# Kernel tuning notes

Measured on AMD Instinct MI355X. Metric: run time of the kernel, lower is better.

The kernel has to match this reference:

```python
import jax, jax.numpy as jnp
from jax import lax
import numpy as np

EPS = 1e-5

def _bn(y, g, b):
    # train-mode batchnorm over (B, H, W) per channel, biased variance (torch default)
    m = y.mean(axis=(0, 2, 3), keepdims=True)
    v = y.var(axis=(0, 2, 3), keepdims=True)
    return (y - m) * lax.rsqrt(v + EPS) * g[None, :, None, None] + b[None, :, None, None]

def _pool13(y):
    # max_pool2d kernel (13,1), stride (13,1); torch truncates the remainder
    B, Ch, L, C = y.shape
    L2 = (L // 13) * 13
    return y[:, :, :L2, :].reshape(B, Ch, L // 13, 13, C).max(axis=3)

def _stagenet(x, w1, b1, w2, b2, g1, be1, w3, b3, g2, be2, wl, bl):
    # x: (B, T=3000, C) -> (B, 100)
    B = x.shape[0]
    y = jnp.einsum('btc,oc->bot', x, w1) + b1[None, :, None]   # spatial conv across channels
    y = y.transpose(0, 2, 1)[:, None]                          # (B,1,T,C)
    y = lax.conv_general_dilated(y, w2, (1, 1), 'VALID', dimension_numbers=('NCHW', 'OIHW', 'NCHW')) + b2[None, :, None, None]
    y = _pool13(_bn(jax.nn.relu(y), g1, be1))                  # (B,16,227,C)
    y = lax.conv_general_dilated(y, w3, (1, 1), 'VALID', dimension_numbers=('NCHW', 'OIHW', 'NCHW')) + b3[None, :, None, None]
    y = _pool13(_bn(jax.nn.relu(y), g2, be2))                  # (B,16,13,C)
    return y.reshape(B, -1) @ wl.T + bl                        # (B,100)

def _gru_last(xs, wih, whh, bih, bhh):
    # xs: (B, S, D) -> final hidden state (B, H); torch gate order r, z, n
    h0 = jnp.zeros((xs.shape[0], whh.shape[1]), xs.dtype)
    def step(h, x):
        gi = x @ wih.T + bih
        gh = h @ whh.T + bhh
        ir, iz, inn = jnp.split(gi, 3, axis=-1)
        hr, hz, hnn = jnp.split(gh, 3, axis=-1)
        r = jax.nn.sigmoid(ir + hr)
        z = jax.nn.sigmoid(iz + hz)
        n = jnp.tanh(inn + r * hnn)
        return (1.0 - z) * n + z * h, None
    hT, _ = lax.scan(step, h0, xs.transpose(1, 0, 2))
    return hT

def setup_inputs() -> dict:
    key = jax.random.key(0)
    ks = jax.random.split(key, 16)
    B, Np, Nb, T, C, H = 16, 16, 10, 3000, 2, 100
    s = 0.1
    f32 = jnp.float32
    return {
        'Xc': jax.random.normal(ks[0], (B, Np, T, C), f32),
        'Xp': jax.random.normal(ks[1], (B, Np, T, C), f32),
        'Xb': jax.random.normal(ks[2], (B, Np, Nb, T, C), f32),
        'sn_w1': jax.random.normal(ks[3], (C, C), f32) * s,
        'sn_b1': jnp.zeros((C,), f32),
        'sn_w2': jax.random.normal(ks[4], (16, 1, 50, 1), f32) * s,
        'sn_b2': jnp.zeros((16,), f32),
        'sn_g1': jnp.ones((16,), f32),
        'sn_be1': jnp.zeros((16,), f32),
        'sn_w3': jax.random.normal(ks[5], (16, 16, 50, 1), f32) * s,
        'sn_b3': jnp.zeros((16,), f32),
        'sn_g2': jnp.ones((16,), f32),
        'sn_be2': jnp.zeros((16,), f32),
        'sn_wl': jax.random.normal(ks[6], (H, 16 * 13 * C), f32) * s,
        'sn_bl': jnp.zeros((H,), f32),
        'gru_wih': jax.random.normal(ks[7], (3 * H, H), f32) * s,
        'gru_whh': jax.random.normal(ks[8], (3 * H, H), f32) * s,
        'gru_bih': jnp.zeros((3 * H,), f32),
        'gru_bhh': jnp.zeros((3 * H,), f32),
        'bilin_w': jax.random.normal(ks[9], (Np, H, H), f32) * s,
    }

def reference(Xc, Xp, Xb, sn_w1, sn_b1, sn_w2, sn_b2, sn_g1, sn_be1, sn_w3, sn_b3, sn_g2, sn_be2, sn_wl, sn_bl, gru_wih, gru_whh, gru_bih, gru_bhh, bilin_w):
    sn = lambda x: _stagenet(x, sn_w1, sn_b1, sn_w2, sn_b2, sn_g1, sn_be1, sn_w3, sn_b3, sn_g2, sn_be2, sn_wl, sn_bl)
    B, Np, Nb, T, C = Xb.shape
    # each original stagenet call sees one window with batch B (BN stats per call) -> vmap over windows
    xb = jax.vmap(sn)(Xb.transpose(1, 2, 0, 3, 4).reshape(Np * Nb, B, T, C))
    xb = xb.reshape(Np, Nb, B, -1).transpose(2, 0, 1, 3)            # (B,Np,Nb,100)
    xc = jax.vmap(sn)(Xc.transpose(1, 0, 2, 3)).transpose(1, 0, 2)  # (B,S,100)
    xp = jax.vmap(sn)(Xp.transpose(1, 0, 2, 3)).transpose(1, 0, 2)  # (B,Np,100)
    hn = _gru_last(xc, gru_wih, gru_whh, gru_bih, gru_bhh)          # (B,100)
    cand = jnp.concatenate([xp[:, :, None, :], xb], axis=2)         # (B,Np,Nb+1,100)
    # per-step bilinear scoring: replaces the triple nested loop of nn.Bilinear calls
    return jnp.einsum('bh,phc,bpsc->bps', hn, bilin_w, cand)        # (B,16,11)
```

## Files before the change

kernel.cpp:

```cpp
#include <hip/hip_runtime.h>
#include <hip/hip_bf16.h>


#define NSEQ 3072
#define CNT1 94432.0f
#define CNT2 5696.0f

__global__ __launch_bounds__(256) void k0_prep(
    const float* __restrict__ wl, const float* __restrict__ w3,
    const float* __restrict__ wih, const float* __restrict__ whh,
    float* __restrict__ wlT, float* __restrict__ w3T,
    float* __restrict__ wihT, float* __restrict__ whhT)
{
    int i = blockIdx.x * 256 + threadIdx.x;
    if (i < 41600) { int h = i / 416, c = i - h * 416; wlT[c * 100 + h] = wl[i]; }
    if (i < 12800) { int co = i / 800, r = i - co * 800; int ci = r / 50, k = r - ci * 50;
                     w3T[(ci * 50 + k) * 16 + co] = w3[i]; }
    if (i < 30000) { int j = i / 100, c = i - j * 100;
                     wihT[c * 300 + j] = wih[i]; whhT[c * 300 + j] = whh[i]; }
}

__global__ __launch_bounds__(256) void k1(
    const float* __restrict__ Xc, const float* __restrict__ Xp, const float* __restrict__ Xb,
    const float* __restrict__ w1, const float* __restrict__ b1,
    const float* __restrict__ w2, const float* __restrict__ b2,
    const float* __restrict__ g1,
    float* __restrict__ pooled1, float* __restrict__ bp1)
{
    const int s = blockIdx.x;
    const int g = s >> 4, b = s & 15;
    const float* x;
    if (g < 160)      { int p = g / 10, nb = g - p * 10; x = Xb + (size_t)((b * 16 + p) * 10 + nb) * 6000; }
    else if (g < 176) { int p = g - 160; x = Xc + (size_t)(b * 16 + p) * 6000; }
    else              { int p = g - 176; x = Xp + (size_t)(b * 16 + p) * 6000; }

    __shared__ float u[6000];
    __shared__ float w2s[800];
    __shared__ float red[512];
    const int tid = threadIdx.x;

    for (int i = tid; i < 800; i += 256) w2s[i] = w2[i];
    float w100 = w1[0], w101 = w1[1], w110 = w1[2], w111 = w1[3];
    float b10 = b1[0], b11 = b1[1];
    for (int t = tid; t < 3000; t += 256) {
        float x0 = x[t * 2], x1 = x[t * 2 + 1];
        u[t * 2]     = fmaf(x1, w101, fmaf(x0, w100, b10));
        u[t * 2 + 1] = fmaf(x1, w111, fmaf(x0, w110, b11));
    }
    __syncthreads();

    const int pair = tid & 31, ch = pair >> 1, col = pair & 1, w8 = tid >> 5;
    float wk[50];
    #pragma unroll
    for (int k = 0; k < 50; ++k) wk[k] = w2s[ch * 50 + k];
    const float bias = b2[ch];
    const bool useMax = (g1[ch] >= 0.0f);

    float lsum = 0.0f, lsq = 0.0f;
    #pragma unroll 1
    for (int w = w8; w < 227; w += 8) {
        const int t0 = w * 13;
        float acc[13];
        #pragma unroll
        for (int j = 0; j < 13; ++j) acc[j] = bias;
        #pragma unroll
        for (int tk = 0; tk < 62; ++tk) {
            float uv = u[(t0 + tk) * 2 + col];
            const int jlo = (tk > 49) ? (tk - 49) : 0;
            const int jhi = (tk < 12) ? tk : 12;
            #pragma unroll
            for (int j = 0; j < 13; ++j)
                if (j >= jlo && j <= jhi) acc[j] = fmaf(uv, wk[tk - j], acc[j]);
        }
        float sel = useMax ? -1e30f : 1e30f;
        #pragma unroll
        for (int j = 0; j < 13; ++j) {
            float r = fmaxf(acc[j], 0.0f);
            lsum += r; lsq = fmaf(r, r, lsq);
            sel = useMax ? fmaxf(sel, r) : fminf(sel, r);
        }
        pooled1[(size_t)s * 7264 + (size_t)w * 32 + pair] = sel;
    }

    red[tid] = lsum;
    __syncthreads();
    float partial_sq = lsq;
    if (tid < 16) {
        float a = 0.0f;
        for (int t = 0; t < 16; ++t) { int idx = (t >> 1) * 32 + tid * 2 + (t & 1); a += red[idx]; }
        bp1[(s * 16 + tid) * 2 + 0] = a;
    }
    __syncthreads();
    red[tid] = partial_sq;
    __syncthreads();
    if (tid < 16) {
        float q = 0.0f;
        for (int t = 0; t < 16; ++t) { int idx = (t >> 1) * 32 + tid * 2 + (t & 1); q += red[idx]; }
        bp1[(s * 16 + tid) * 2 + 1] = q;
    }
}

__global__ __launch_bounds__(512) void k2(
    const float* __restrict__ pooled1, const float* __restrict__ bp1,
    const float* __restrict__ g1, const float* __restrict__ be1,
    const float* __restrict__ w3T, const float* __restrict__ b3,
    const float* __restrict__ g2,
    float* __restrict__ pooled2, float* __restrict__ bp2)
{
    const int s = blockIdx.x, g = s >> 4;
    __shared__ float in2[7424];
    __shared__ float w3b[800];
    __shared__ float sc1[16], sh1[16];
    __shared__ float red[1024];
    const int tid = threadIdx.x;

    if (tid < 16) {
        float sum = 0.0f, sq = 0.0f;
        for (int sb = 0; sb < 16; ++sb) {
            const float* pp = &bp1[((g * 16 + sb) * 16 + tid) * 2];
            sum += pp[0]; sq += pp[1];
        }
        float m = sum * (1.0f / CNT1);
        float v = sq * (1.0f / CNT1) - m * m;
        float scv = g1[tid] * rsqrtf(v + 1e-5f);
        sc1[tid] = scv; sh1[tid] = be1[tid] - m * scv;
    }
    for (int i = tid; i < 7424; i += 512) in2[i] = 0.0f;
    __syncthreads();
    for (int idx = tid; idx < 7264; idx += 512) {
        int w = idx >> 5, pr = idx & 31, ch = pr >> 1, cl = pr & 1;
        in2[(cl * 16 + ch) * 232 + w] = fmaf(pooled1[(size_t)s * 7264 + idx], sc1[ch], sh1[ch]);
    }

    const int pair = tid & 31, co = pair >> 1, col = pair & 1, wslot = tid >> 5;
    const bool active = (wslot < 14);
    const int t0 = wslot * 13;
    float acc[13];
    const float bias = b3[co];
    #pragma unroll
    for (int j = 0; j < 13; ++j) acc[j] = bias;

    for (int ci = 0; ci < 16; ++ci) {
        __syncthreads();
        for (int i = tid; i < 800; i += 512) w3b[i] = w3T[ci * 800 + i];
        __syncthreads();
        if (active) {
            float wk[50];
            #pragma unroll
            for (int k = 0; k < 50; ++k) wk[k] = w3b[k * 16 + co];
            const float* ip = &in2[(col * 16 + ci) * 232 + t0];
            #pragma unroll
            for (int tk = 0; tk < 62; ++tk) {
                float uv = ip[tk];
                const int jlo = (tk > 49) ? (tk - 49) : 0;
                const int jhi = (tk < 12) ? tk : 12;
                #pragma unroll
                for (int j = 0; j < 13; ++j)
                    if (j >= jlo && j <= jhi) acc[j] = fmaf(uv, wk[tk - j], acc[j]);
            }
        }
    }

    float lsum = 0.0f, lsq = 0.0f;
    const bool useMax2 = (g2[co] >= 0.0f);
    float sel = useMax2 ? -1e30f : 1e30f;
    if (active) {
        const int base = wslot * 13;
        #pragma unroll
        for (int j = 0; j < 13; ++j) {
            if (base + j < 178) {
                float r = fmaxf(acc[j], 0.0f);
                lsum += r; lsq = fmaf(r, r, lsq);
                sel = useMax2 ? fmaxf(sel, r) : fminf(sel, r);
            }
        }
        if (wslot < 13) pooled2[(size_t)s * 416 + co * 26 + wslot * 2 + col] = sel;
    }
    red[tid] = lsum; red[512 + tid] = lsq;
    __syncthreads();
    if (tid < 16) {
        float a = 0.0f, q = 0.0f;
        for (int t = 0; t < 32; ++t) {
            int idx = (t >> 1) * 32 + tid * 2 + (t & 1);
            a += red[idx]; q += red[512 + idx];
        }
        bp2[(s * 16 + tid) * 2 + 0] = a;
        bp2[(s * 16 + tid) * 2 + 1] = q;
    }
}

__global__ __launch_bounds__(128) void k3(
    const float* __restrict__ bp2, const float* __restrict__ g2, const float* __restrict__ be2,
    const float* __restrict__ pooled2, const float* __restrict__ wlT,
    const float* __restrict__ bl, float* __restrict__ feat)
{
    const int s = blockIdx.x, g = s >> 4;
    const int tid = threadIdx.x;
    __shared__ float sc[16], sh[16], z[416];
    if (tid < 16) {
        float sum = 0.0f, sq = 0.0f;
        for (int sb = 0; sb < 16; ++sb) {
            const float* pp = &bp2[((g * 16 + sb) * 16 + tid) * 2];
            sum += pp[0]; sq += pp[1];
        }
        float m = sum * (1.0f / CNT2);
        float v = sq * (1.0f / CNT2) - m * m;
        float scv = g2[tid] * rsqrtf(v + 1e-5f);
        sc[tid] = scv; sh[tid] = be2[tid] - m * scv;
    }
    __syncthreads();
    for (int i = tid; i < 416; i += 128) {
        int co = i / 26;
        z[i] = fmaf(pooled2[(size_t)s * 416 + i], sc[co], sh[co]);
    }
    __syncthreads();
    for (int h = tid; h < 100; h += 128) {
        float acc = bl[h];
        for (int i = 0; i < 416; ++i) acc = fmaf(wlT[i * 100 + h], z[i], acc);
        feat[(size_t)s * 100 + h] = acc;
    }
}

__global__ __launch_bounds__(128) void k4a(
    const float* __restrict__ feat, const float* __restrict__ wihT,
    const float* __restrict__ bih, float* __restrict__ gi)
{
    const int b = blockIdx.x >> 4, p = blockIdx.x & 15;
    const int tid = threadIdx.x;
    __shared__ float xr[100];
    if (tid < 100) xr[tid] = feat[(size_t)((160 + p) * 16 + b) * 100 + tid];
    __syncthreads();
    for (int j = tid; j < 300; j += 128) {
        float acc = bih[j];
        for (int i = 0; i < 100; ++i) acc = fmaf(xr[i], wihT[i * 300 + j], acc);
        gi[(size_t)(b * 16 + p) * 300 + j] = acc;
    }
}

__global__ __launch_bounds__(320) void k4b(
    const float* __restrict__ gi, const float* __restrict__ whhT,
    const float* __restrict__ bhh, float* __restrict__ hn)
{
    const int b = blockIdx.x;
    const int tid = threadIdx.x;
    __shared__ float h[100], ga[300], gb[300];
    if (tid < 100) h[tid] = 0.0f;
    __syncthreads();
    for (int p = 0; p < 16; ++p) {
        if (tid < 300) {
            float acc = bhh[tid];
            for (int i = 0; i < 100; ++i) acc = fmaf(h[i], whhT[i * 300 + tid], acc);
            gb[tid] = acc;
            ga[tid] = gi[(size_t)(b * 16 + p) * 300 + tid];
        }
        __syncthreads();
        if (tid < 100) {
            float r  = 1.0f / (1.0f + expf(-(ga[tid] + gb[tid])));
            float zz = 1.0f / (1.0f + expf(-(ga[100 + tid] + gb[100 + tid])));
            float n  = tanhf(ga[200 + tid] + r * gb[200 + tid]);
            h[tid] = (1.0f - zz) * n + zz * h[tid];
        }
        __syncthreads();
    }
    if (tid < 100) hn[b * 100 + tid] = h[tid];
}

__global__ __launch_bounds__(128) void k5(
    const float* __restrict__ hn, const float* __restrict__ bw,
    const float* __restrict__ feat, float* __restrict__ out)
{
    const int b = blockIdx.x >> 4, p = blockIdx.x & 15;
    const int tid = threadIdx.x;
    __shared__ float hs[100], ts[100];
    if (tid < 100) hs[tid] = hn[b * 100 + tid];
    __syncthreads();
    if (tid < 100) {
        float acc = 0.0f;
        for (int hh = 0; hh < 100; ++hh)
            acc = fmaf(hs[hh], bw[(size_t)(p * 100 + hh) * 100 + tid], acc);
        ts[tid] = acc;
    }
    __syncthreads();
    if (tid < 11) {
        const float* cr = (tid == 0)
            ? &feat[(size_t)((176 + p) * 16 + b) * 100]
            : &feat[(size_t)((p * 10 + tid - 1) * 16 + b) * 100];
        float acc = 0.0f;
        for (int hh = 0; hh < 100; ++hh) acc = fmaf(ts[hh], cr[hh], acc);
        out[(b * 16 + p) * 11 + tid] = acc;
    }
}

extern "C" void kernel_launch(void* const* d_in, const int* in_sizes, int n_in,
                              void* d_out, int out_size, void* d_ws, size_t ws_size,
                              hipStream_t stream) {
    (void)in_sizes; (void)n_in; (void)out_size; (void)ws_size;
    const float* Xc  = (const float*)d_in[0];
    const float* Xp  = (const float*)d_in[1];
    const float* Xb  = (const float*)d_in[2];
    const float* w1  = (const float*)d_in[3];
    const float* b1  = (const float*)d_in[4];
    const float* w2  = (const float*)d_in[5];
    const float* b2  = (const float*)d_in[6];
    const float* g1  = (const float*)d_in[7];
    const float* be1 = (const float*)d_in[8];
    const float* w3  = (const float*)d_in[9];
    const float* b3  = (const float*)d_in[10];
    const float* g2  = (const float*)d_in[11];
    const float* be2 = (const float*)d_in[12];
    const float* wl  = (const float*)d_in[13];
    const float* bl  = (const float*)d_in[14];
    const float* wih = (const float*)d_in[15];
    const float* whh = (const float*)d_in[16];
    const float* bih = (const float*)d_in[17];
    const float* bhh = (const float*)d_in[18];
    const float* bw  = (const float*)d_in[19];

    float* ws      = (float*)d_ws;
    float* bp1     = ws;
    float* bp2     = ws + 98304;
    float* wlT     = ws + 196608;
    float* w3T     = ws + 238208;
    float* wihT    = ws + 251008;
    float* whhT    = ws + 281008;
    float* gi      = ws + 311008;
    float* hn      = ws + 387808;
    float* feat    = ws + 389408;
    float* pooled2 = ws + 696608;
    float* pooled1 = ws + 1974560;

    k0_prep<<<163, 256, 0, stream>>>(wl, w3, wih, whh, wlT, w3T, wihT, whhT);
    k1<<<NSEQ, 256, 0, stream>>>(Xc, Xp, Xb, w1, b1, w2, b2, g1, pooled1, bp1);
    k2<<<NSEQ, 512, 0, stream>>>(pooled1, bp1, g1, be1, w3T, b3, g2, pooled2, bp2);
    k3<<<NSEQ, 128, 0, stream>>>(bp2, g2, be2, pooled2, wlT, bl, feat);
    k4a<<<256, 128, 0, stream>>>(feat, wihT, bih, gi);
    k4b<<<16, 320, 0, stream>>>(gi, whhT, bhh, hn);
    k5<<<256, 128, 0, stream>>>(hn, bw, feat, (float*)d_out);
}
```

Before: 762.5 us.

## Double-buffer conv3 weights, trim idle warps, vectorize input loads in conv kernels

In k2 the per-input-channel weight slice is now double-buffered in shared memory, so the next slice is prefetched while the current one is used. This removes one of the two barriers per channel iteration. The block shrinks from 512 to 448 threads, dropping the two idle warps, and only the padding tail of the input buffer is zeroed instead of all of it. k1 loads and writes its channel-mix input with float4, and both kernels pin the weight registers with empty asm statements to keep the compiler from rematerializing them.

```diff
diff --git a/kernel.cpp b/kernel.cpp
--- a/kernel.cpp
+++ b/kernel.cpp
@@ -34,7 +34,7 @@
     else if (g < 176) { int p = g - 160; x = Xc + (size_t)(b * 16 + p) * 6000; }
     else              { int p = g - 176; x = Xp + (size_t)(b * 16 + p) * 6000; }
 
-    __shared__ float u[6000];
+    __shared__ __align__(16) float u[6000];
     __shared__ float w2s[800];
     __shared__ float red[512];
     const int tid = threadIdx.x;
@@ -42,10 +42,14 @@
     for (int i = tid; i < 800; i += 256) w2s[i] = w2[i];
     float w100 = w1[0], w101 = w1[1], w110 = w1[2], w111 = w1[3];
     float b10 = b1[0], b11 = b1[1];
-    for (int t = tid; t < 3000; t += 256) {
-        float x0 = x[t * 2], x1 = x[t * 2 + 1];
-        u[t * 2]     = fmaf(x1, w101, fmaf(x0, w100, b10));
-        u[t * 2 + 1] = fmaf(x1, w111, fmaf(x0, w110, b11));
+    for (int t4 = tid; t4 < 1500; t4 += 256) {
+        float4 xv = ((const float4*)x)[t4];
+        float4 uv;
+        uv.x = fmaf(xv.y, w101, fmaf(xv.x, w100, b10));
+        uv.y = fmaf(xv.y, w111, fmaf(xv.x, w110, b11));
+        uv.z = fmaf(xv.w, w101, fmaf(xv.z, w100, b10));
+        uv.w = fmaf(xv.w, w111, fmaf(xv.z, w110, b11));
+        ((float4*)u)[t4] = uv;
     }
     __syncthreads();
 
@@ -53,6 +57,8 @@
     float wk[50];
     #pragma unroll
     for (int k = 0; k < 50; ++k) wk[k] = w2s[ch * 50 + k];
+    #pragma unroll
+    for (int k = 0; k < 50; ++k) asm volatile("" : "+v"(wk[k]));
     const float bias = b2[ch];
     const bool useMax = (g1[ch] >= 0.0f);
 
@@ -100,7 +106,7 @@
     }
 }
 
-__global__ __launch_bounds__(512) void k2(
+__global__ __launch_bounds__(448) void k2(
     const float* __restrict__ pooled1, const float* __restrict__ bp1,
     const float* __restrict__ g1, const float* __restrict__ be1,
     const float* __restrict__ w3T, const float* __restrict__ b3,
@@ -109,9 +115,9 @@
 {
     const int s = blockIdx.x, g = s >> 4;
     __shared__ float in2[7424];
-    __shared__ float w3b[800];
+    __shared__ float w3b[2][800];
     __shared__ float sc1[16], sh1[16];
-    __shared__ float red[1024];
+    __shared__ float red[896];
     const int tid = threadIdx.x;
 
     if (tid < 16) {
@@ -125,46 +131,48 @@
         float scv = g1[tid] * rsqrtf(v + 1e-5f);
         sc1[tid] = scv; sh1[tid] = be1[tid] - m * scv;
     }
-    for (int i = tid; i < 7424; i += 512) in2[i] = 0.0f;
-    __syncthreads();
-    for (int idx = tid; idx < 7264; idx += 512) {
+    if (tid < 160) { int row = tid / 5, w = 227 + tid % 5; in2[row * 232 + w] = 0.0f; }
+    for (int i = tid; i < 800; i += 448) w3b[0][i] = w3T[i];
+    __syncthreads();
+    for (int idx = tid; idx < 7264; idx += 448) {
         int w = idx >> 5, pr = idx & 31, ch = pr >> 1, cl = pr & 1;
         in2[(cl * 16 + ch) * 232 + w] = fmaf(pooled1[(size_t)s * 7264 + idx], sc1[ch], sh1[ch]);
     }
 
     const int pair = tid & 31, co = pair >> 1, col = pair & 1, wslot = tid >> 5;
-    const bool active = (wslot < 14);
     const int t0 = wslot * 13;
     float acc[13];
     const float bias = b3[co];
     #pragma unroll
     for (int j = 0; j < 13; ++j) acc[j] = bias;
+    __syncthreads();
 
     for (int ci = 0; ci < 16; ++ci) {
+        const int cur = ci & 1;
+        if (ci < 15)
+            for (int i = tid; i < 800; i += 448) w3b[cur ^ 1][i] = w3T[(ci + 1) * 800 + i];
+        float wk[50];
+        #pragma unroll
+        for (int k = 0; k < 50; ++k) wk[k] = w3b[cur][k * 16 + co];
+        #pragma unroll
+        for (int k = 0; k < 50; ++k) asm volatile("" : "+v"(wk[k]));
+        const float* ip = &in2[(col * 16 + ci) * 232 + t0];
+        #pragma unroll
+        for (int tk = 0; tk < 62; ++tk) {
+            float uv = ip[tk];
+            const int jlo = (tk > 49) ? (tk - 49) : 0;
+            const int jhi = (tk < 12) ? tk : 12;
+            #pragma unroll
+            for (int j = 0; j < 13; ++j)
+                if (j >= jlo && j <= jhi) acc[j] = fmaf(uv, wk[tk - j], acc[j]);
+        }
         __syncthreads();
-        for (int i = tid; i < 800; i += 512) w3b[i] = w3T[ci * 800 + i];
-        __syncthreads();
-        if (active) {
-            float wk[50];
-            #pragma unroll
-            for (int k = 0; k < 50; ++k) wk[k] = w3b[k * 16 + co];
-            const float* ip = &in2[(col * 16 + ci) * 232 + t0];
-            #pragma unroll
-            for (int tk = 0; tk < 62; ++tk) {
-                float uv = ip[tk];
-                const int jlo = (tk > 49) ? (tk - 49) : 0;
-                const int jhi = (tk < 12) ? tk : 12;
-                #pragma unroll
-                for (int j = 0; j < 13; ++j)
-                    if (j >= jlo && j <= jhi) acc[j] = fmaf(uv, wk[tk - j], acc[j]);
-            }
-        }
     }
 
     float lsum = 0.0f, lsq = 0.0f;
     const bool useMax2 = (g2[co] >= 0.0f);
     float sel = useMax2 ? -1e30f : 1e30f;
-    if (active) {
+    {
         const int base = wslot * 13;
         #pragma unroll
         for (int j = 0; j < 13; ++j) {
@@ -176,13 +184,13 @@
         }
         if (wslot < 13) pooled2[(size_t)s * 416 + co * 26 + wslot * 2 + col] = sel;
     }
-    red[tid] = lsum; red[512 + tid] = lsq;
+    red[tid] = lsum; red[448 + tid] = lsq;
     __syncthreads();
     if (tid < 16) {
         float a = 0.0f, q = 0.0f;
-        for (int t = 0; t < 32; ++t) {
+        for (int t = 0; t < 28; ++t) {
             int idx = (t >> 1) * 32 + tid * 2 + (t & 1);
-            a += red[idx]; q += red[512 + idx];
+            a += red[idx]; q += red[448 + idx];
         }
         bp2[(s * 16 + tid) * 2 + 0] = a;
         bp2[(s * 16 + tid) * 2 + 1] = q;
@@ -331,7 +339,7 @@
 
     k0_prep<<<163, 256, 0, stream>>>(wl, w3, wih, whh, wlT, w3T, wihT, whhT);
     k1<<<NSEQ, 256, 0, stream>>>(Xc, Xp, Xb, w1, b1, w2, b2, g1, pooled1, bp1);
-    k2<<<NSEQ, 512, 0, stream>>>(pooled1, bp1, g1, be1, w3T, b3, g2, pooled2, bp2);
+    k2<<<NSEQ, 448, 0, stream>>>(pooled1, bp1, g1, be1, w3T, b3, g2, pooled2, bp2);
     k3<<<NSEQ, 128, 0, stream>>>(bp2, g2, be2, pooled2, wlT, bl, feat);
     k4a<<<256, 128, 0, stream>>>(feat, wihT, bih, gi);
     k4b<<<16, 320, 0, stream>>>(gi, whhT, bhh, hn);
```

Measured after the change: 804.4 us. +5.5%, slower.
